# Performance work log

Measured on AMD Instinct MI355X. Metric: run time of the kernel, lower is better.

The kernel has to match this reference:

```python
import jax, jax.numpy as jnp
import numpy as np

T, B, D, H, A = 256, 512, 128, 128, 8
RUN_COUNT = 1000

def _orth(k, shape, scale):
    w = jax.random.normal(k, shape, jnp.float32)
    q, r = jnp.linalg.qr(w)
    q = q * jnp.sign(jnp.diag(r))[None, :]
    return scale * q

def setup_inputs() -> dict:
    key = jax.random.key(0)
    ks = jax.random.split(key, 12)
    return {
        'hidden': jnp.zeros((B, H), jnp.float32),
        'obs': jax.random.normal(ks[0], (T, B, D), jnp.float32),
        'dones': (jax.random.randint(ks[1], (T, B), 0, 10) == 0),
        'mean_obs': jax.random.normal(ks[2], (D,), jnp.float32) * 0.1,
        'welford_S': jax.random.uniform(ks[3], (D,), jnp.float32) * RUN_COUNT,
        'running_count': RUN_COUNT,
        'W_emb': _orth(ks[4], (D, H), float(np.sqrt(2.0))), 'b_emb': jnp.zeros((H,), jnp.float32),
        'Wi': jax.random.normal(ks[5], (H, 3 * H), jnp.float32) / np.sqrt(H),
        'Wh': jax.random.normal(ks[6], (H, 3 * H), jnp.float32) / np.sqrt(H),
        'bh': jnp.zeros((3 * H,), jnp.float32),
        'W_act': _orth(ks[7], (H, H), 2.0), 'b_act': jnp.zeros((H,), jnp.float32),
        'W_alpha': _orth(ks[8], (H, A), 0.01), 'b_alpha': jnp.zeros((A,), jnp.float32),
        'W_beta': _orth(ks[9], (H, A), 0.01), 'b_beta': jnp.zeros((A,), jnp.float32),
    }

def _welford(M0, S0, count0, xs):
    # sequential Welford update over stacked rows, as in the original lax.scan
    def step(carry, x):
        M, S, c = carry
        c = c + 1.0
        M_new = M + (x - M) / c
        S_new = S + (x - M) * (x - M_new)
        return (M_new, S_new, c), None
    (M, S, c), _ = jax.lax.scan(step, (M0, S0, jnp.asarray(count0, jnp.float32)), xs)
    return M, S, c

def reference(hidden, obs, dones, mean_obs, welford_S, running_count,
              W_emb, b_emb, Wi, Wh, bh, W_act, b_act, W_alpha, b_alpha, W_beta, b_beta):
    # --- running-stat normalization (running_count > 0 branch) ---
    stacked = obs.reshape(-1, obs.shape[-1])  # [T*B, D]
    M, S, c = _welford(mean_obs, welford_S, running_count, stacked)
    var = S / (c - 1.0)
    obs_n = (obs - M) / (jnp.sqrt(var) + 1e-8)
    # --- embedding MLP ---
    emb = jax.nn.relu(obs_n @ W_emb + b_emb)  # [T, B, H]
    # --- GRU scan over time; precompute input-side gate projections (no input bias, flax GRUCell) ---
    xg = emb @ Wi  # [T, B, 3H]
    def gru_step(h, inp):
        x3, reset = inp
        h = jnp.where(reset[:, None], 0.0, h)  # reset carry where done
        hg = h @ Wh + bh
        xr, xz, xn = jnp.split(x3, 3, axis=-1)
        hr, hz, hn = jnp.split(hg, 3, axis=-1)
        r = jax.nn.sigmoid(xr + hr)
        z = jax.nn.sigmoid(xz + hz)
        n = jnp.tanh(xn + r * hn)
        h_new = (1.0 - z) * n + z * h
        return h_new, h_new
    h_last, ys = jax.lax.scan(gru_step, hidden, (xg, dones))  # ys: [T, B, H]
    # --- policy heads ---
    act = jax.nn.relu(ys @ W_act + b_act)
    alpha = jax.nn.softplus(act @ W_alpha + b_alpha) + 1.0
    beta = jax.nn.softplus(act @ W_beta + b_beta) + 1.0
    return h_last, alpha, beta, M, S
```

## Files before the change

### kernel.cpp

```cpp
#include <hip/hip_runtime.h>

#define T_DIM 256
#define B_DIM 512
#define D_DIM 128
#define H_DIM 128
#define A_DIM 8
#define N_ROWS (T_DIM*B_DIM)
#define NT (N_ROWS/16)
#define NWIN 8
#define WLEN 32
#define LOG2E 1.4426950408889634f

typedef __attribute__((ext_vector_type(4))) float f32x4;
typedef __attribute__((ext_vector_type(8))) short bf16x8;
typedef __attribute__((ext_vector_type(4))) short bf16x4;
typedef __attribute__((ext_vector_type(8))) _Float16 f16x8;
typedef __attribute__((ext_vector_type(4))) unsigned u32x4;
typedef __attribute__((ext_vector_type(2))) unsigned u32x2;

#define OFF_PSUM   0ull
#define OFF_PSQ    1048576ull
#define OFF_STATM  2097152ull
#define OFF_STATI  2097664ull
#define OFF_WEMB   2098176ull
#define OFF_WI     2130944ull
#define OFF_WH     2229248ull
#define OFF_WACT   2425856ull
#define OFF_WHEAD  2458624ull
#define OFF_TLO    2462720ull
#define OFF_UH     2464768ull
#define OFF_XG     4194304ull
#define OFF_YS     104857600ull

#define OUT_H      0
#define OUT_ALPHA  65536
#define OUT_BETA   1114112
#define OUT_M      2162688
#define OUT_S      2162816

__device__ inline short f2bf(float x){
  union { float f; unsigned u; } v; v.f = x;
  unsigned r = v.u + 0x7FFFu + ((v.u>>16)&1u);
  return (short)(r>>16);
}
__device__ inline float bf2f(short h){
  union { unsigned u; float f; } v; v.u = ((unsigned)(unsigned short)h)<<16; return v.f;
}

__device__ inline int swz(int row, int col){ return row*136 + col; }

__device__ inline unsigned cvtpk_bf16(float lo, float hi){
  unsigned r;
  asm("v_cvt_pk_bf16_f32 %0, %1, %2" : "=v"(r) : "v"(lo), "v"(hi));
  return r;
}

__global__ __launch_bounds__(256)
void k_fused(const float* __restrict__ obs,
             double* __restrict__ psum, double* __restrict__ psq,
             const unsigned char* __restrict__ dones,
             int* __restrict__ tlo, unsigned char* __restrict__ usehid,
             const float* __restrict__ W_emb, const float* __restrict__ Wi,
             const float* __restrict__ Wh,    const float* __restrict__ W_act,
             const float* __restrict__ W_al,  const float* __restrict__ W_be,
             short* __restrict__ Bemb, short* __restrict__ BWi,
             short* __restrict__ BWh,  short* __restrict__ Bact,
             short* __restrict__ Bhead){
  __shared__ double ls[256], lq[256];
  __shared__ int red[512];
  int bx = blockIdx.x, tid = threadIdx.x;

  if (bx < 1024){
    int col = tid & 127; int rh = tid >> 7;
    double s = 0.0, q = 0.0;
    for (int r = bx*2 + rh; r < N_ROWS; r += 2048){
      float v = obs[(size_t)r*D_DIM + col];
      s += (double)v; q += (double)v*(double)v;
    }
    ls[tid]=s; lq[tid]=q; __syncthreads();
    if (rh==0){
      psum[(size_t)bx*128 + col] = ls[tid] + ls[tid+128];
      psq [(size_t)bx*128 + col] = lq[tid] + lq[tid+128];
    }
    return;
  }
  if (bx < 1032){
    int k = bx - 1024;
    #pragma unroll
    for (int h=0; h<2; h++){
      int b = tid + h*256;
      int t0 = 0, uh = 1;
      if (k > 0){
        for (int t = WLEN*k; t >= 0; t--){
          if (dones[(size_t)t*B_DIM + b]){ t0 = t; uh = 0; break; }
        }
      }
      usehid[k*B_DIM + b] = (unsigned char)uh;
      red[b] = t0;
    }
    __syncthreads();
    if (tid < 32){
      int m = red[tid*16];
      #pragma unroll
      for (int i=1;i<16;i++) m = min(m, red[tid*16+i]);
      tlo[k*32 + tid] = m;
    }
    return;
  }
  int gidx = (bx-1032)*256 + tid;
  if (gidx >= 133120) return;
  if (gidx >= 131072){
    int idx = gidx - 131072;
    int j = idx & 7, lane = (idx>>3)&63, kb = (idx>>9)&3;
    int k = kb*32 + (lane>>4)*8 + j;
    int n = lane & 15;
    float wv = (n<8) ? W_al[(size_t)k*8 + n] : W_be[(size_t)k*8 + (n-8)];
    Bhead[idx] = f2bf(wv);
    return;
  }
  const float* src; short* dst; int C; int fmt; int idx;
  if (gidx < 16384)      { src=W_emb; dst=Bemb; C=128; fmt=0; idx=gidx; }
  else if (gidx < 65536) { src=Wi;    dst=BWi;  C=384; fmt=0; idx=gidx-16384; }
  else if (gidx < 114688){ src=Wh;    dst=BWh;  C=384; fmt=1; idx=gidx-65536; }
  else                   { src=W_act; dst=Bact; C=128; fmt=0; idx=gidx-114688; }
  int j = idx & 7, lane = (idx>>3)&63, kb = (idx>>9)&3, ct = idx>>11;
  int k = kb*32 + (lane>>4)*8 + j;
  int n = ct*16 + (lane&15);
  float wv = src[(size_t)k*C + n];
  short h;
  if (fmt==0) h = f2bf(wv);
  else {
    wv *= (n < 256) ? LOG2E : (2.f*LOG2E);
    union { _Float16 hf; short s; } u; u.hf = (_Float16)wv; h = u.s;
  }
  dst[idx] = h;
}

__global__ __launch_bounds__(1024) void k_stats(const double* __restrict__ psum,
                                                const double* __restrict__ psq,
                                                const float* __restrict__ mean_obs,
                                                const float* __restrict__ welfS,
                                                const int* __restrict__ runcnt,
                                                float* __restrict__ outM, float* __restrict__ outS,
                                                float* __restrict__ wsM,  float* __restrict__ wsI){
  int tid = threadIdx.x; int col = tid & 127; int seg = tid >> 7;
  double s=0.0, q=0.0;
  for (int b=seg; b<1024; b+=8){ s += psum[(size_t)b*128+col]; q += psq[(size_t)b*128+col]; }
  __shared__ double ls[1024], lq[1024];
  ls[tid]=s; lq[tid]=q; __syncthreads();
  if (seg==0){
    for (int b=1;b<8;b++){ s += ls[b*128+col]; q += lq[b*128+col]; }
    double c0 = (double)runcnt[0];
    double Nn = (double)N_ROWS;
    double n  = c0 + Nn;
    double M0 = (double)mean_obs[col], S0 = (double)welfS[col];
    double mb = s / Nn;
    double delta = mb - M0;
    double M = M0 + delta * Nn / n;
    double M2b = q - Nn*mb*mb;
    double S = S0 + M2b + delta*delta*c0*Nn/n;
    double var = S / (n - 1.0);
    float inv = (float)(1.0/(sqrt(var)+1e-8));
    outM[col] = (float)M; outS[col] = (float)S;
    wsM[col]  = (float)M; wsI[col]  = inv;
  }
}

__global__ __launch_bounds__(256) void k_embxg(const float* __restrict__ obs,
                                               const float* __restrict__ wsM,
                                               const float* __restrict__ wsI,
                                               const short* __restrict__ Bemb,
                                               const float* __restrict__ b_emb,
                                               const short* __restrict__ BWi,
                                               const float* __restrict__ bh,
                                               short* __restrict__ xgpk){
  int tid=threadIdx.x, w=tid>>6, lane=tid&63, q=lane>>4, l=lane&15;
  __shared__ __align__(16) short Wlds[16384];
  __shared__ __align__(16) short scratch[4][16*136];

  short* Lw = &scratch[w][0];
  int rt0 = blockIdx.x*16 + w*4;

  {
    u32x4* dst = (u32x4*)Wlds;
    const u32x4* src = (const u32x4*)Bemb;
    #pragma unroll
    for (int i=0;i<8;i++) dst[tid + i*256] = src[tid + i*256];
  }
  __syncthreads();

  bf16x8 a2[4][4];
  #pragma unroll
  for (int tt=0; tt<4; tt++){
    int rt = rt0 + tt;
    int r0 = rt*16;
    {
      int row = lane>>2, c0 = (lane&3)*32;
      const float* op = obs + (size_t)(r0+row)*D_DIM + c0;
      #pragma unroll
      for (int it=0; it<8; it++){
        f32x4 o = *(const f32x4*)(op + it*4);
        f32x4 m = *(const f32x4*)(wsM + c0 + it*4);
        f32x4 iv= *(const f32x4*)(wsI + c0 + it*4);
        bf16x4 v;
        v[0]=f2bf((o[0]-m[0])*iv[0]); v[1]=f2bf((o[1]-m[1])*iv[1]);
        v[2]=f2bf((o[2]-m[2])*iv[2]); v[3]=f2bf((o[3]-m[3])*iv[3]);
        *(bf16x4*)&Lw[swz(row, c0+it*4)] = v;
      }
    }
    asm volatile("s_waitcnt lgkmcnt(0)" ::: "memory");
    bf16x8 A[4];
    #pragma unroll
    for (int kb=0;kb<4;kb++) A[kb] = *(const bf16x8*)&Lw[swz(l, kb*32+q*8)];
    asm volatile("s_waitcnt lgkmcnt(0)" ::: "memory");
    #pragma unroll
    for (int ct=0; ct<8; ct++){
      f32x4 acc = {0.f,0.f,0.f,0.f};
      #pragma unroll
      for (int kb=0;kb<4;kb++)
        acc = __builtin_amdgcn_mfma_f32_16x16x32_bf16(A[kb],
                *(const bf16x8*)&Wlds[((ct*4+kb)*64+lane)*8], acc, 0,0,0);
      float bb = b_emb[ct*16 + l];
      #pragma unroll
      for (int r2=0;r2<4;r2++){
        float e = acc[r2] + bb; e = e>0.f ? e : 0.f;
        Lw[swz(q*4+r2, ct*16+l)] = f2bf(e);
      }
    }
    asm volatile("s_waitcnt lgkmcnt(0)" ::: "memory");
    #pragma unroll
    for (int kb=0;kb<4;kb++) a2[tt][kb] = *(const bf16x8*)&Lw[swz(l, kb*32+q*8)];
    asm volatile("s_waitcnt lgkmcnt(0)" ::: "memory");
  }
  __syncthreads();

  u32x2* xg8 = (u32x2*)xgpk;
  for (int g=0; g<3; g++){
    {
      u32x4* dst = (u32x4*)Wlds;
      const u32x4* src = (const u32x4*)BWi + (size_t)g*2048;
      #pragma unroll
      for (int i=0;i<8;i++) dst[tid + i*256] = src[tid + i*256];
    }
    __syncthreads();
    float sc = (g<2) ? LOG2E : (2.f*LOG2E);
    #pragma unroll
    for (int tt=0; tt<4; tt++){
      int rt = rt0 + tt;
      #pragma unroll
      for (int j=0; j<8; j++){
        int ct = g*8 + j;
        f32x4 acc = {0.f,0.f,0.f,0.f};
        #pragma unroll
        for (int kb=0;kb<4;kb++)
          acc = __builtin_amdgcn_mfma_f32_16x16x32_bf16(a2[tt][kb],
                  *(const bf16x8*)&Wlds[((j*4+kb)*64+lane)*8], acc, 0,0,0);
        int col = ct*16 + l;
        float bv = (g<2) ? bh[col] : 0.f;
        u32x2 pv;
        pv[0] = cvtpk_bf16((acc[0]+bv)*sc, (acc[1]+bv)*sc);
        pv[1] = cvtpk_bf16((acc[2]+bv)*sc, (acc[3]+bv)*sc);
        xg8[((size_t)rt*24 + ct)*64 + lane] = pv;
      }
    }
    if (g < 2) __syncthreads();
  }
}

#define LDB(g,kb) __builtin_bit_cast(f16x8, pw4[(((g)*8+w)*4+(kb))*64+lane])
__global__
__attribute__((amdgpu_flat_work_group_size(512,512)))
__attribute__((amdgpu_waves_per_eu(2,2)))
void k_gru(const float* __restrict__ hidden,
           const unsigned char* __restrict__ dones,
           const short* __restrict__ xgpk,
           const short* __restrict__ BWh,
           const float* __restrict__ bh,
           const int* __restrict__ tlo,
           const unsigned char* __restrict__ usehid,
           short* __restrict__ yspk,
           float* __restrict__ h_last,
           const short* __restrict__ Bact,
           const float* __restrict__ b_act,
           const short* __restrict__ Bhead,
           const float* __restrict__ b_alpha,
           const float* __restrict__ b_beta,
           float* __restrict__ alpha,
           float* __restrict__ beta){
  int tid=threadIdx.x, w=tid>>6, lane=tid&63, q=lane>>4, l=lane&15;
  int kk = blockIdx.x >> 5, bt = blockIdx.x & 31;
  int t_out0 = kk*WLEN;
  int t_end  = t_out0 + WLEN;
  int t_start = tlo[kk*32 + bt];

  __shared__ __align__(16) char Ubytes[8*16*136*2];

  const u32x4* pw4 = (const u32x4*)BWh;
  f16x8 B00 = LDB(0,0), B01 = LDB(0,1), B02 = LDB(0,2), B03 = LDB(0,3);
  f16x8 B10 = LDB(1,0), B11 = LDB(1,1), B12 = LDB(1,2), B13 = LDB(1,3);
  f16x8 B20 = LDB(2,0), B21 = LDB(2,1), B22 = LDB(2,2), B23 = LDB(2,3);

  float bh2c = bh[2*128 + w*16 + l] * (2.f*LOG2E);

  float hv[4];
  #pragma unroll
  for (int r2=0;r2<4;r2++){
    int b = bt*16 + q*4 + r2;
    hv[r2] = usehid[kk*B_DIM + b] ? hidden[(size_t)b*H_DIM + w*16 + l] : 0.f;
  }

  const bf16x4* xgt = (const bf16x4*)xgpk + (((size_t)t_start*32 + bt)*24 + w)*64 + lane;
  const unsigned char* dnp = dones + (size_t)t_start*B_DIM + bt*16 + q*4;
  bf16x4* yst = (bf16x4*)yspk + (((size_t)t_start*32 + bt)*8 + w)*64 + lane;

  bf16x4 xr_c = xgt[0], xz_c = xgt[512], xn_c = xgt[1024];
  unsigned dn_c = *(const unsigned*)dnp;
  { int a1 = (t_start+1 < t_end) ? 1 : 0; xgt += (size_t)a1*49152; dnp += a1*B_DIM; }
  bf16x4 xr_n = xgt[0], xz_n = xgt[512], xn_n = xgt[1024];
  unsigned dn_n = *(const unsigned*)dnp;

  _Float16* hA = (_Float16*)Ubytes;
  _Float16* hB = (_Float16*)Ubytes + 16*136;
  const int wo = q*4*136 + w*16 + l;
  const int ro = l*136 + q*8;

  for (int t = t_start; t < t_end; t++){
    #pragma unroll
    for (int r2=0;r2<4;r2++){
      float hvv = ((dn_c >> (r2*8)) & 255u) ? 0.f : hv[r2];
      hv[r2] = hvv;
      hA[wo + r2*136] = (_Float16)hvv;
    }
    asm volatile("s_waitcnt lgkmcnt(0)" ::: "memory");
    __builtin_amdgcn_s_barrier();
    asm volatile("" ::: "memory");

    int a2 = (t+2 < t_end) ? 1 : 0;
    xgt += (size_t)a2 * 49152;
    dnp += a2 * B_DIM;
    bf16x4 xr_2 = xgt[0], xz_2 = xgt[512], xn_2 = xgt[1024];
    unsigned dn_2 = *(const unsigned*)dnp;

    f16x8 A0 = *(const f16x8*)(hA + ro +  0);
    f16x8 A1 = *(const f16x8*)(hA + ro + 32);
    f16x8 A2 = *(const f16x8*)(hA + ro + 64);
    f16x8 A3 = *(const f16x8*)(hA + ro + 96);

    f32x4 acc0 = {0.f,0.f,0.f,0.f}, acc1 = {0.f,0.f,0.f,0.f}, acc2 = {0.f,0.f,0.f,0.f};
    acc0 = __builtin_amdgcn_mfma_f32_16x16x32_f16(A0, B00, acc0, 0,0,0);
    acc1 = __builtin_amdgcn_mfma_f32_16x16x32_f16(A0, B10, acc1, 0,0,0);
    acc2 = __builtin_amdgcn_mfma_f32_16x16x32_f16(A0, B20, acc2, 0,0,0);
    acc0 = __builtin_amdgcn_mfma_f32_16x16x32_f16(A1, B01, acc0, 0,0,0);
    acc1 = __builtin_amdgcn_mfma_f32_16x16x32_f16(A1, B11, acc1, 0,0,0);
    acc2 = __builtin_amdgcn_mfma_f32_16x16x32_f16(A1, B21, acc2, 0,0,0);
    acc0 = __builtin_amdgcn_mfma_f32_16x16x32_f16(A2, B02, acc0, 0,0,0);
    acc1 = __builtin_amdgcn_mfma_f32_16x16x32_f16(A2, B12, acc1, 0,0,0);
    acc2 = __builtin_amdgcn_mfma_f32_16x16x32_f16(A2, B22, acc2, 0,0,0);
    acc0 = __builtin_amdgcn_mfma_f32_16x16x32_f16(A3, B03, acc0, 0,0,0);
    acc1 = __builtin_amdgcn_mfma_f32_16x16x32_f16(A3, B13, acc1, 0,0,0);
    acc2 = __builtin_amdgcn_mfma_f32_16x16x32_f16(A3, B23, acc2, 0,0,0);

    #pragma unroll
    for (int r2=0;r2<4;r2++){
      float xr = bf2f(xr_c[r2]), xz = bf2f(xz_c[r2]), xn = bf2f(xn_c[r2]);
      float rg = __builtin_amdgcn_rcpf(1.f + __builtin_amdgcn_exp2f(-(xr + acc0[r2])));
      float zg = __builtin_amdgcn_rcpf(1.f + __builtin_amdgcn_exp2f(-(xz + acc1[r2])));
      float e2 = __builtin_amdgcn_exp2f(xn + rg*(acc2[r2] + bh2c));
      float ng = 1.f - 2.f*__builtin_amdgcn_rcpf(e2 + 1.f);
      hv[r2] = ng + zg*(hv[r2] - ng);
    }
    if (t >= t_out0){
      u32x2 pv;
      pv[0] = cvtpk_bf16(hv[0], hv[1]);
      pv[1] = cvtpk_bf16(hv[2], hv[3]);
      *(u32x2*)yst = pv;
    }
    yst += 16384;
    xr_c = xr_n; xz_c = xz_n; xn_c = xn_n; dn_c = dn_n;
    xr_n = xr_2; xz_n = xz_2; xn_n = xn_2; dn_n = dn_2;
    _Float16* tmp = hA; hA = hB; hB = tmp;
  }

  if (kk == NWIN-1){
    #pragma unroll
    for (int r2=0;r2<4;r2++)
      h_last[(size_t)(bt*16+q*4+r2)*H_DIM + w*16 + l] = hv[r2];
  }

  asm volatile("s_waitcnt vmcnt(0)" ::: "memory");
  __syncthreads();

  short* Lw = (short*)Ubytes + (size_t)w*(16*136);
  const bf16x8* BA  = (const bf16x8*)Bact;
  const bf16x8* BHd = (const bf16x8*)Bhead;
  const bf16x4* ys4 = (const bf16x4*)yspk;

  for (int j=0; j<4; j++){
    int t = t_out0 + w*4 + j;
    size_t rt = (size_t)t*32 + bt;
    #pragma unroll
    for (int ct=0; ct<8; ct++){
      bf16x4 v = ys4[(rt*8+ct)*64+lane];
      #pragma unroll
      for (int r2=0;r2<4;r2++) Lw[swz(q*4+r2, ct*16+l)] = v[r2];
    }
    asm volatile("s_waitcnt lgkmcnt(0)" ::: "memory");
    bf16x8 A[4];
    #pragma unroll
    for (int kb=0;kb<4;kb++) A[kb] = *(const bf16x8*)&Lw[swz(l, kb*32+q*8)];
    asm volatile("s_waitcnt lgkmcnt(0)" ::: "memory");
    #pragma unroll
    for (int ct=0;ct<8;ct++){
      f32x4 acc = {0.f,0.f,0.f,0.f};
      #pragma unroll
      for (int kb=0;kb<4;kb++)
        acc = __builtin_amdgcn_mfma_f32_16x16x32_bf16(A[kb], BA[(ct*4+kb)*64+lane], acc, 0,0,0);
      int col = ct*16 + l;
      float bb = b_act[col];
      #pragma unroll
      for (int r2=0;r2<4;r2++){
        float e = acc[r2] + bb; e = e>0.f ? e : 0.f;
        Lw[swz(q*4+r2, col)] = f2bf(e);
      }
    }
    asm volatile("s_waitcnt lgkmcnt(0)" ::: "memory");
    bf16x8 A2[4];
    #pragma unroll
    for (int kb=0;kb<4;kb++) A2[kb] = *(const bf16x8*)&Lw[swz(l, kb*32+q*8)];
    asm volatile("s_waitcnt lgkmcnt(0)" ::: "memory");
    f32x4 acc = {0.f,0.f,0.f,0.f};
    #pragma unroll
    for (int kb=0;kb<4;kb++)
      acc = __builtin_amdgcn_mfma_f32_16x16x32_bf16(A2[kb], BHd[kb*64+lane], acc, 0,0,0);
    float bb = (l<8) ? b_alpha[l] : b_beta[l-8];
    float* dst = (l<8) ? alpha : beta;
    int cc = (l<8) ? l : l-8;
    #pragma unroll
    for (int r2=0;r2<4;r2++){
      float u = acc[r2] + bb;
      float e = __builtin_amdgcn_exp2f(-fabsf(u)*LOG2E);
      float sp = fmaxf(u,0.f) + 0.6931471805599453f*__builtin_amdgcn_logf(1.f + e);
      dst[(rt*16 + q*4 + r2)*8 + cc] = sp + 1.f;
    }
  }
}

extern "C" void kernel_launch(void* const* d_in, const int* in_sizes, int n_in,
                              void* d_out, int out_size, void* d_ws, size_t ws_size,
                              hipStream_t stream){
  const float* hidden   = (const float*)d_in[0];
  const float* obs      = (const float*)d_in[1];
  const unsigned char* dones = (const unsigned char*)d_in[2];
  const float* mean_obs = (const float*)d_in[3];
  const float* welfS    = (const float*)d_in[4];
  const int*   runcnt   = (const int*)d_in[5];
  const float* W_emb = (const float*)d_in[6];
  const float* b_emb = (const float*)d_in[7];
  const float* Wi    = (const float*)d_in[8];
  const float* Wh    = (const float*)d_in[9];
  const float* bh    = (const float*)d_in[10];
  const float* W_act = (const float*)d_in[11];
  const float* b_act = (const float*)d_in[12];
  const float* W_al  = (const float*)d_in[13];
  const float* b_al  = (const float*)d_in[14];
  const float* W_be  = (const float*)d_in[15];
  const float* b_be  = (const float*)d_in[16];
  float* out = (float*)d_out;
  char*  ws  = (char*)d_ws;

  double* psum = (double*)(ws + OFF_PSUM);
  double* psq  = (double*)(ws + OFF_PSQ);
  float*  wsM  = (float*)(ws + OFF_STATM);
  float*  wsI  = (float*)(ws + OFF_STATI);
  short*  Bemb = (short*)(ws + OFF_WEMB);
  short*  BWi  = (short*)(ws + OFF_WI);
  short*  BWh  = (short*)(ws + OFF_WH);
  short*  Bact = (short*)(ws + OFF_WACT);
  short*  Bhead= (short*)(ws + OFF_WHEAD);
  int*    tlo  = (int*)(ws + OFF_TLO);
  unsigned char* uh = (unsigned char*)(ws + OFF_UH);
  short*  xgpk = (short*)(ws + OFF_XG);
  short*  yspk = (short*)(ws + OFF_YS);

  k_fused<<<1552,256,0,stream>>>(obs, psum, psq, dones, tlo, uh,
                                 W_emb, Wi, Wh, W_act, W_al, W_be,
                                 Bemb, BWi, BWh, Bact, Bhead);
  k_stats<<<1,1024,0,stream>>>(psum, psq, mean_obs, welfS, runcnt,
                               out+OUT_M, out+OUT_S, wsM, wsI);
  k_embxg<<<512,256,0,stream>>>(obs, wsM, wsI, Bemb, b_emb, BWi, bh, xgpk);
  k_gru<<<NWIN*32,512,0,stream>>>(hidden, dones, xgpk, BWh, bh, tlo, uh,
                                  yspk, out + OUT_H,
                                  Bact, b_act, Bhead, b_al, b_be,
                                  out + OUT_ALPHA, out + OUT_BETA);
}
```

Measured before the change: 539.1 us.

## Split GRU batch tiles in half and move policy heads to separate kernel

The GRU kernel now handles 8 batch rows per block instead of 16, doubling the grid to 512 blocks. Each block still runs 16-row MFMAs, with the upper half of lanes duplicating or zero-padding rows. Occupancy is raised to 4 waves per EU and the per-window tlo reduction now works on groups of 8. The action and alpha/beta head computation moves out of the GRU kernel into a new k_heads kernel that stages its weights in LDS. The intent is more parallelism on the latency-bound recurrence, at the cost of redundant MFMA work and an extra launch that re-reads ys.

```diff
diff --git a/kernel.cpp b/kernel.cpp
--- a/kernel.cpp
+++ b/kernel.cpp
@@ -99,11 +99,11 @@
       red[b] = t0;
     }
     __syncthreads();
-    if (tid < 32){
-      int m = red[tid*16];
-      #pragma unroll
-      for (int i=1;i<16;i++) m = min(m, red[tid*16+i]);
-      tlo[k*32 + tid] = m;
+    if (tid < 64){
+      int m = red[tid*8];
+      #pragma unroll
+      for (int i=1;i<8;i++) m = min(m, red[tid*8+i]);
+      tlo[k*64 + tid] = m;
     }
     return;
   }
@@ -270,7 +270,7 @@
 #define LDB(g,kb) __builtin_bit_cast(f16x8, pw4[(((g)*8+w)*4+(kb))*64+lane])
 __global__
 __attribute__((amdgpu_flat_work_group_size(512,512)))
-__attribute__((amdgpu_waves_per_eu(2,2)))
+__attribute__((amdgpu_waves_per_eu(4,4)))
 void k_gru(const float* __restrict__ hidden,
            const unsigned char* __restrict__ dones,
            const short* __restrict__ xgpk,
@@ -279,21 +279,16 @@
            const int* __restrict__ tlo,
            const unsigned char* __restrict__ usehid,
            short* __restrict__ yspk,
-           float* __restrict__ h_last,
-           const short* __restrict__ Bact,
-           const float* __restrict__ b_act,
-           const short* __restrict__ Bhead,
-           const float* __restrict__ b_alpha,
-           const float* __restrict__ b_beta,
-           float* __restrict__ alpha,
-           float* __restrict__ beta){
+           float* __restrict__ h_last){
   int tid=threadIdx.x, w=tid>>6, lane=tid&63, q=lane>>4, l=lane&15;
-  int kk = blockIdx.x >> 5, bt = blockIdx.x & 31;
+  int kk = blockIdx.x >> 6, bt8 = blockIdx.x & 63;
+  int half = bt8 & 1, rtb = bt8 >> 1;
+  int elane = lane ^ (half<<5);
   int t_out0 = kk*WLEN;
   int t_end  = t_out0 + WLEN;
-  int t_start = tlo[kk*32 + bt];
-
-  __shared__ __align__(16) char Ubytes[8*16*136*2];
+  int t_start = tlo[kk*64 + bt8];
+
+  __shared__ __align__(16) _Float16 hF[2][16*136];
 
   const u32x4* pw4 = (const u32x4*)BWh;
   f16x8 B00 = LDB(0,0), B01 = LDB(0,1), B02 = LDB(0,2), B03 = LDB(0,3);
@@ -305,13 +300,16 @@
   float hv[4];
   #pragma unroll
   for (int r2=0;r2<4;r2++){
-    int b = bt*16 + q*4 + r2;
-    hv[r2] = usehid[kk*B_DIM + b] ? hidden[(size_t)b*H_DIM + w*16 + l] : 0.f;
-  }
-
-  const bf16x4* xgt = (const bf16x4*)xgpk + (((size_t)t_start*32 + bt)*24 + w)*64 + lane;
-  const unsigned char* dnp = dones + (size_t)t_start*B_DIM + bt*16 + q*4;
-  bf16x4* yst = (bf16x4*)yspk + (((size_t)t_start*32 + bt)*8 + w)*64 + lane;
+    hv[r2] = 0.f;
+    if (q < 2){
+      int b = bt8*8 + q*4 + r2;
+      hv[r2] = usehid[kk*B_DIM + b] ? hidden[(size_t)b*H_DIM + w*16 + l] : 0.f;
+    }
+  }
+
+  const bf16x4* xgt = (const bf16x4*)xgpk + (((size_t)t_start*32 + rtb)*24 + w)*64 + elane;
+  const unsigned char* dnp = dones + (size_t)t_start*B_DIM + bt8*8 + (q&1)*4;
+  bf16x4* yst = (bf16x4*)yspk + (((size_t)t_start*32 + rtb)*8 + w)*64 + elane;
 
   bf16x4 xr_c = xgt[0], xz_c = xgt[512], xn_c = xgt[1024];
   unsigned dn_c = *(const unsigned*)dnp;
@@ -319,8 +317,8 @@
   bf16x4 xr_n = xgt[0], xz_n = xgt[512], xn_n = xgt[1024];
   unsigned dn_n = *(const unsigned*)dnp;
 
-  _Float16* hA = (_Float16*)Ubytes;
-  _Float16* hB = (_Float16*)Ubytes + 16*136;
+  _Float16* hA = &hF[0][0];
+  _Float16* hB = &hF[1][0];
   const int wo = q*4*136 + w*16 + l;
   const int ro = l*136 + q*8;
 
@@ -369,7 +367,7 @@
       float ng = 1.f - 2.f*__builtin_amdgcn_rcpf(e2 + 1.f);
       hv[r2] = ng + zg*(hv[r2] - ng);
     }
-    if (t >= t_out0){
+    if (t >= t_out0 && lane < 32){
       u32x2 pv;
       pv[0] = cvtpk_bf16(hv[0], hv[1]);
       pv[1] = cvtpk_bf16(hv[2], hv[3]);
@@ -381,23 +379,41 @@
     _Float16* tmp = hA; hA = hB; hB = tmp;
   }
 
-  if (kk == NWIN-1){
+  if (kk == NWIN-1 && q < 2){
     #pragma unroll
     for (int r2=0;r2<4;r2++)
-      h_last[(size_t)(bt*16+q*4+r2)*H_DIM + w*16 + l] = hv[r2];
-  }
-
-  asm volatile("s_waitcnt vmcnt(0)" ::: "memory");
+      h_last[(size_t)(bt8*8+q*4+r2)*H_DIM + w*16 + l] = hv[r2];
+  }
+}
+
+__global__ __launch_bounds__(256) void k_heads(const short* __restrict__ yspk,
+                                               const short* __restrict__ Bact,
+                                               const float* __restrict__ b_act,
+                                               const short* __restrict__ Bhead,
+                                               const float* __restrict__ b_alpha,
+                                               const float* __restrict__ b_beta,
+                                               float* __restrict__ alpha,
+                                               float* __restrict__ beta){
+  int tid=threadIdx.x, w=tid>>6, lane=tid&63, q=lane>>4, l=lane&15;
+  __shared__ __align__(16) short Wlds[16384];
+  __shared__ __align__(16) short Hlds[2048];
+  __shared__ __align__(16) short scratch[4][16*136];
+  short* Lw = &scratch[w][0];
+  size_t rt0 = (size_t)blockIdx.x*16 + w*4;
+
+  {
+    u32x4* dst = (u32x4*)Wlds;
+    const u32x4* src = (const u32x4*)Bact;
+    #pragma unroll
+    for (int i=0;i<8;i++) dst[tid + i*256] = src[tid + i*256];
+    ((u32x4*)Hlds)[tid] = ((const u32x4*)Bhead)[tid];
+  }
   __syncthreads();
 
-  short* Lw = (short*)Ubytes + (size_t)w*(16*136);
-  const bf16x8* BA  = (const bf16x8*)Bact;
-  const bf16x8* BHd = (const bf16x8*)Bhead;
   const bf16x4* ys4 = (const bf16x4*)yspk;
-
-  for (int j=0; j<4; j++){
-    int t = t_out0 + w*4 + j;
-    size_t rt = (size_t)t*32 + bt;
+  #pragma unroll
+  for (int tt=0; tt<4; tt++){
+    size_t rt = rt0 + tt;
     #pragma unroll
     for (int ct=0; ct<8; ct++){
       bf16x4 v = ys4[(rt*8+ct)*64+lane];
@@ -414,7 +430,8 @@
       f32x4 acc = {0.f,0.f,0.f,0.f};
       #pragma unroll
       for (int kb=0;kb<4;kb++)
-        acc = __builtin_amdgcn_mfma_f32_16x16x32_bf16(A[kb], BA[(ct*4+kb)*64+lane], acc, 0,0,0);
+        acc = __builtin_amdgcn_mfma_f32_16x16x32_bf16(A[kb],
+                *(const bf16x8*)&Wlds[((ct*4+kb)*64+lane)*8], acc, 0,0,0);
       int col = ct*16 + l;
       float bb = b_act[col];
       #pragma unroll
@@ -431,7 +448,8 @@
     f32x4 acc = {0.f,0.f,0.f,0.f};
     #pragma unroll
     for (int kb=0;kb<4;kb++)
-      acc = __builtin_amdgcn_mfma_f32_16x16x32_bf16(A2[kb], BHd[kb*64+lane], acc, 0,0,0);
+      acc = __builtin_amdgcn_mfma_f32_16x16x32_bf16(A2[kb],
+              *(const bf16x8*)&Hlds[(kb*64+lane)*8], acc, 0,0,0);
     float bb = (l<8) ? b_alpha[l] : b_beta[l-8];
     float* dst = (l<8) ? alpha : beta;
     int cc = (l<8) ? l : l-8;
@@ -488,8 +506,8 @@
   k_stats<<<1,1024,0,stream>>>(psum, psq, mean_obs, welfS, runcnt,
                                out+OUT_M, out+OUT_S, wsM, wsI);
   k_embxg<<<512,256,0,stream>>>(obs, wsM, wsI, Bemb, b_emb, BWi, bh, xgpk);
-  k_gru<<<NWIN*32,512,0,stream>>>(hidden, dones, xgpk, BWh, bh, tlo, uh,
-                                  yspk, out + OUT_H,
-                                  Bact, b_act, Bhead, b_al, b_be,
-                                  out + OUT_ALPHA, out + OUT_BETA);
-}
+  k_gru<<<NWIN*64,512,0,stream>>>(hidden, dones, xgpk, BWh, bh, tlo, uh,
+                                  yspk, out + OUT_H);
+  k_heads<<<512,256,0,stream>>>(yspk, Bact, b_act, Bhead, b_al, b_be,
+                                out + OUT_ALPHA, out + OUT_BETA);
+}
```

Measured after the change: 619.5 us. 1.15x slower.
